# Performance work log

Measured on AMD Instinct MI355X. Metric: run time of the kernel, lower is better.

## Reference

```python
import jax, jax.numpy as jnp
import numpy as np

OUT_F, IN_F = 4096, 4096
BLOCK = 64  # bitsandbytes NF4 block size

# NF4 code table (bitsandbytes): 16 quantile levels of a standard normal, scaled to [-1, 1]
NF4_CODE = jnp.array([
    -1.0, -0.6961928009986877, -0.5250730514526367, -0.39491748809814453,
    -0.28444138169288635, -0.18477343022823334, -0.09105003625154495, 0.0,
    0.07958029955625534, 0.16093020141124725, 0.24611230194568634, 0.33791524171829224,
    0.44070982933044434, 0.5626170039176941, 0.7229568362236023, 1.0,
], dtype=jnp.float32)


def dequantize_nf4(packed, absmax):
    # packed: [OUT_F*IN_F//2] int values in [0,256); two 4-bit indices per byte (high nibble first)
    hi = (packed >> 4) & 0xF
    lo = packed & 0xF
    idx = jnp.stack([hi, lo], axis=-1).reshape(-1)           # [OUT_F*IN_F]
    vals = NF4_CODE[idx]                                      # lookup
    vals = vals.reshape(-1, BLOCK) * absmax[:, None]          # per-block scale
    return vals.reshape(OUT_F, IN_F)


def setup_inputs() -> dict:
    key = jax.random.key(0)
    k1, k2, k3, k4 = jax.random.split(key, 4)
    x = jax.random.normal(k1, (4, 2048, IN_F), dtype=jnp.float32)
    packed_weight = jax.random.randint(k2, (OUT_F * IN_F // 2,), 0, 256, dtype=jnp.int32)
    absmax = jax.random.uniform(k3, (OUT_F * IN_F // BLOCK,), dtype=jnp.float32)
    bias = jax.random.normal(k4, (OUT_F,), dtype=jnp.float32)
    return {"x": x, "packed_weight": packed_weight, "absmax": absmax, "bias": bias}


def reference(x, packed_weight, absmax, bias):
    weight = dequantize_nf4(packed_weight, absmax)            # [OUT_F, IN_F]
    # F.linear: x @ W^T + b
    return jnp.einsum('bsi,oi->bso', x, weight) + bias
```

## Files before the change

### kernel.cpp

```cpp
#include <hip/hip_runtime.h>
#include <hip/hip_bf16.h>
#include <stdint.h>

#define IN_F   4096
#define OUT_F  4096
#define MROWS  8192
#define NT     64

typedef __bf16 bf16x8 __attribute__((ext_vector_type(8)));
typedef float  f32x4  __attribute__((ext_vector_type(4)));
typedef unsigned short ushort8v __attribute__((ext_vector_type(8)));

__device__ __constant__ float NF4_TAB[16] = {
    -1.0f, -0.6961928009986877f, -0.5250730514526367f, -0.39491748809814453f,
    -0.28444138169288635f, -0.18477343022823334f, -0.09105003625154495f, 0.0f,
    0.07958029955625534f, 0.16093020141124725f, 0.24611230194568634f, 0.33791524171829224f,
    0.44070982933044434f, 0.5626170039176941f, 0.7229568362236023f, 1.0f,
};

__device__ __forceinline__ unsigned short f2bf_rne(float f) {
    unsigned u = __builtin_bit_cast(unsigned, f);
    return (unsigned short)((u + 0x7FFFu + ((u >> 16) & 1u)) >> 16);
}

__global__ __launch_bounds__(256) void prep_kernel(
        const float* __restrict__ x, const int* __restrict__ packed,
        const float* __restrict__ absmax,
        unsigned short* __restrict__ Wb, unsigned short* __restrict__ Xb) {
    __shared__ float tab[16];
    if (threadIdx.x < 16) tab[threadIdx.x] = NF4_TAB[threadIdx.x];
    __syncthreads();

    const int bid = blockIdx.x;
    if (bid < 512) {
        const int ngroups = OUT_F * IN_F / 8;
        const int stride = 512 * 256;
        for (int g = bid * 256 + threadIdx.x; g < ngroups; g += stride) {
            int4 pv = reinterpret_cast<const int4*>(packed)[g];
            float am = absmax[g >> 3];
            ushort8v o;
            o[0] = f2bf_rne(tab[(pv.x >> 4) & 0xF] * am);
            o[1] = f2bf_rne(tab[ pv.x       & 0xF] * am);
            o[2] = f2bf_rne(tab[(pv.y >> 4) & 0xF] * am);
            o[3] = f2bf_rne(tab[ pv.y       & 0xF] * am);
            o[4] = f2bf_rne(tab[(pv.z >> 4) & 0xF] * am);
            o[5] = f2bf_rne(tab[ pv.z       & 0xF] * am);
            o[6] = f2bf_rne(tab[(pv.w >> 4) & 0xF] * am);
            o[7] = f2bf_rne(tab[ pv.w       & 0xF] * am);
            *reinterpret_cast<ushort8v*>(&Wb[(size_t)g * 8]) = o;
        }
    } else {
        const int ngroups = MROWS * IN_F / 8;
        const int stride = 1536 * 256;
        for (int g = (bid - 512) * 256 + threadIdx.x; g < ngroups; g += stride) {
            float4 v0 = reinterpret_cast<const float4*>(x)[2 * g];
            float4 v1 = reinterpret_cast<const float4*>(x)[2 * g + 1];
            ushort8v o;
            o[0] = f2bf_rne(v0.x); o[1] = f2bf_rne(v0.y);
            o[2] = f2bf_rne(v0.z); o[3] = f2bf_rne(v0.w);
            o[4] = f2bf_rne(v1.x); o[5] = f2bf_rne(v1.y);
            o[6] = f2bf_rne(v1.z); o[7] = f2bf_rne(v1.w);
            *reinterpret_cast<ushort8v*>(&Xb[(size_t)g * 8]) = o;
        }
    }
}

#define GLOAD16(gp, lp)                                                        \
    __builtin_amdgcn_global_load_lds(                                          \
        (const __attribute__((address_space(1))) void*)(gp),                   \
        (__attribute__((address_space(3))) void*)(lp), 16, 0, 0)

#define BARF()  asm volatile("s_barrier" ::: "memory")
#define VMW(n)  asm volatile("s_waitcnt vmcnt(" #n ")" ::: "memory")

__global__ __launch_bounds__(512) void gemm256_kernel(
        const unsigned short* __restrict__ A,
        const unsigned short* __restrict__ B,
        const float* __restrict__ bias,
        float* __restrict__ C) {
    __shared__ __align__(16) unsigned short lds[65536];

    const int tid  = threadIdx.x;
    const int lane = tid & 63;
    const int wave = tid >> 6;
    const int wr   = wave >> 2;
    const int wcn  = wave & 3;
    const int lr   = lane & 15;
    const int lg   = lane >> 4;

    const int bid = blockIdx.x;
    const int wg  = (bid & 7) * 64 + (bid >> 3);
    const int bm  = (wg >> 4) << 8;
    const int bn  = (wg & 15) << 8;

    int srow[2], skel[2];
#pragma unroll
    for (int r = 0; r < 2; ++r) {
        int c = tid + r * 512;
        int L = c * 16;
        int sw = L ^ (((L >> 7) & 7) << 4);
        srow[r] = sw >> 6;
        skel[r] = (sw & 63) >> 1;
    }
    const unsigned short* pA0 = A + (size_t)(bm + srow[0]) * IN_F + skel[0];
    const unsigned short* pA1 = A + (size_t)(bm + srow[1]) * IN_F + skel[1];
    const unsigned short* pB0 = B + (size_t)(bn + srow[0]) * IN_F + skel[0];
    const unsigned short* pB1 = B + (size_t)(bn + srow[1]) * IN_F + skel[1];
    const int d0 = tid * 8, d1 = tid * 8 + 4096;

#define STAGE_A(t, kh) do {                                                    \
        int _b = ((t) & 1) * 32768 + (kh) * 8192;                              \
        int _k = (t) * 64 + (kh) * 32;                                         \
        GLOAD16(pA0 + _k, &lds[_b + d0]);                                      \
        GLOAD16(pA1 + _k, &lds[_b + d1]); } while (0)
#define STAGE_B(t, kh) do {                                                    \
        int _b = ((t) & 1) * 32768 + 16384 + (kh) * 8192;                      \
        int _k = (t) * 64 + (kh) * 32;                                         \
        GLOAD16(pB0 + _k, &lds[_b + d0]);                                      \
        GLOAD16(pB1 + _k, &lds[_b + d1]); } while (0)

    const int laneoff = ((lr * 64 + lg * 16) ^ (((lr >> 1) & 7) << 4)) >> 1;
    const int arow = wr * 128;
    const int brow = wcn * 64;

    f32x4  acc[8][4] = {};
    bf16x8 af[4], bfv[4];

#define LOADB(b, kh) do {                                                      \
        int _base = (b) * 32768 + 16384 + (kh) * 8192 + brow * 32 + laneoff;   \
        bfv[0] = *reinterpret_cast<const bf16x8*>(&lds[_base]);                \
        bfv[1] = *reinterpret_cast<const bf16x8*>(&lds[_base + 512]);          \
        bfv[2] = *reinterpret_cast<const bf16x8*>(&lds[_base + 1024]);         \
        bfv[3] = *reinterpret_cast<const bf16x8*>(&lds[_base + 1536]); } while (0)
#define LOADA(b, kh, mq) do {                                                  \
        int _base = (b) * 32768 + (kh) * 8192 + (arow + (mq) * 64) * 32 + laneoff; \
        af[0] = *reinterpret_cast<const bf16x8*>(&lds[_base]);                 \
        af[1] = *reinterpret_cast<const bf16x8*>(&lds[_base + 512]);           \
        af[2] = *reinterpret_cast<const bf16x8*>(&lds[_base + 1024]);          \
        af[3] = *reinterpret_cast<const bf16x8*>(&lds[_base + 1536]); } while (0)

#define MFMA16(mq) do {                                                        \
        __builtin_amdgcn_s_setprio(1);                                         \
        _Pragma("unroll")                                                      \
        for (int mi = 0; mi < 4; ++mi)                                         \
            _Pragma("unroll")                                                  \
            for (int ni = 0; ni < 4; ++ni)                                     \
                acc[(mq) * 4 + mi][ni] = __builtin_amdgcn_mfma_f32_16x16x32_bf16( \
                    af[mi], bfv[ni], acc[(mq) * 4 + mi][ni], 0, 0, 0);         \
        __builtin_amdgcn_s_setprio(0); } while (0)

#define PHASE1(b, S) do { LOADB(b, 0); LOADA(b, 0, 0); S;                      \
        MFMA16(0); BARF(); } while (0)
#define PHASE2(b, S) do { LOADA(b, 0, 1); S;                                   \
        MFMA16(1); BARF(); } while (0)
#define PHASE3(b, S) do { LOADB(b, 1); LOADA(b, 1, 0); S;                      \
        MFMA16(0); BARF(); } while (0)
#define PHASE4(b, S, V) do { LOADA(b, 1, 1); S;                                \
        MFMA16(1); V; BARF(); } while (0)

    STAGE_B(0, 0); STAGE_A(0, 0); STAGE_B(0, 1); STAGE_A(0, 1);
    STAGE_B(1, 0); STAGE_A(1, 0); STAGE_B(1, 1);
    VMW(6);
    BARF();

#pragma unroll 2
    for (int t = 0; t < NT - 2; ++t) {
        const int b = t & 1;
        PHASE1(b, STAGE_A(t + 1, 1));
        PHASE2(b, STAGE_B(t + 2, 0));
        PHASE3(b, STAGE_A(t + 2, 0));
        PHASE4(b, STAGE_B(t + 2, 1), VMW(6));
    }
    PHASE1(0, STAGE_A(NT - 1, 1));
    PHASE2(0, );
    PHASE3(0, );
    PHASE4(0, , VMW(0));
    PHASE1(1, );
    PHASE2(1, );
    PHASE3(1, );
    PHASE4(1, , );

#pragma unroll
    for (int a = 0; a < 8; ++a) {
        const int row0 = bm + wr * 128 + (a >> 2) * 64 + (a & 3) * 16 + lg * 4;
#pragma unroll
        for (int ni = 0; ni < 4; ++ni) {
            const int col = bn + wcn * 64 + ni * 16 + lr;
            const float bs = bias[col];
            float* cp = C + (size_t)row0 * OUT_F + col;
#pragma unroll
            for (int j = 0; j < 4; ++j)
                cp[(size_t)j * OUT_F] = acc[a][ni][j] + bs;
        }
    }
}

extern "C" void kernel_launch(void* const* d_in, const int* in_sizes, int n_in,
                              void* d_out, int out_size, void* d_ws, size_t ws_size,
                              hipStream_t stream) {
    const float* x      = (const float*)d_in[0];
    const int*   packed = (const int*)d_in[1];
    const float* absmax = (const float*)d_in[2];
    const float* bias   = (const float*)d_in[3];
    float* out = (float*)d_out;

    unsigned short* Wb = (unsigned short*)d_ws;
    unsigned short* Xb = Wb + (size_t)OUT_F * IN_F;

    prep_kernel<<<2048, 256, 0, stream>>>(x, packed, absmax, Wb, Xb);
    gemm256_kernel<<<512, 512, 0, stream>>>(Xb, Wb, bias, out);
}
```

Measured before the change: 482.0 us.

## Merge four MFMA phases into two per k-tile with dual A fragment registers

```diff
diff --git a/kernel.cpp b/kernel.cpp
--- a/kernel.cpp
+++ b/kernel.cpp
@@ -124,7 +124,7 @@
     const int brow = wcn * 64;
 
     f32x4  acc[8][4] = {};
-    bf16x8 af[4], bfv[4];
+    bf16x8 af0[4], af1[4], bfv[4];
 
 #define LOADB(b, kh) do {                                                      \
         int _base = (b) * 32768 + 16384 + (kh) * 8192 + brow * 32 + laneoff;   \
@@ -132,53 +132,48 @@
         bfv[1] = *reinterpret_cast<const bf16x8*>(&lds[_base + 512]);          \
         bfv[2] = *reinterpret_cast<const bf16x8*>(&lds[_base + 1024]);         \
         bfv[3] = *reinterpret_cast<const bf16x8*>(&lds[_base + 1536]); } while (0)
-#define LOADA(b, kh, mq) do {                                                  \
+#define LOADA(b, kh, mq, dst) do {                                             \
         int _base = (b) * 32768 + (kh) * 8192 + (arow + (mq) * 64) * 32 + laneoff; \
-        af[0] = *reinterpret_cast<const bf16x8*>(&lds[_base]);                 \
-        af[1] = *reinterpret_cast<const bf16x8*>(&lds[_base + 512]);           \
-        af[2] = *reinterpret_cast<const bf16x8*>(&lds[_base + 1024]);          \
-        af[3] = *reinterpret_cast<const bf16x8*>(&lds[_base + 1536]); } while (0)
-
-#define MFMA16(mq) do {                                                        \
+        dst[0] = *reinterpret_cast<const bf16x8*>(&lds[_base]);                \
+        dst[1] = *reinterpret_cast<const bf16x8*>(&lds[_base + 512]);          \
+        dst[2] = *reinterpret_cast<const bf16x8*>(&lds[_base + 1024]);         \
+        dst[3] = *reinterpret_cast<const bf16x8*>(&lds[_base + 1536]); } while (0)
+
+#define MFMA32() do {                                                          \
         __builtin_amdgcn_s_setprio(1);                                         \
         _Pragma("unroll")                                                      \
         for (int mi = 0; mi < 4; ++mi)                                         \
             _Pragma("unroll")                                                  \
             for (int ni = 0; ni < 4; ++ni)                                     \
-                acc[(mq) * 4 + mi][ni] = __builtin_amdgcn_mfma_f32_16x16x32_bf16( \
-                    af[mi], bfv[ni], acc[(mq) * 4 + mi][ni], 0, 0, 0);         \
+                acc[mi][ni] = __builtin_amdgcn_mfma_f32_16x16x32_bf16(         \
+                    af0[mi], bfv[ni], acc[mi][ni], 0, 0, 0);                   \
+        _Pragma("unroll")                                                      \
+        for (int mi = 0; mi < 4; ++mi)                                         \
+            _Pragma("unroll")                                                  \
+            for (int ni = 0; ni < 4; ++ni)                                     \
+                acc[4 + mi][ni] = __builtin_amdgcn_mfma_f32_16x16x32_bf16(     \
+                    af1[mi], bfv[ni], acc[4 + mi][ni], 0, 0, 0);               \
         __builtin_amdgcn_s_setprio(0); } while (0)
 
-#define PHASE1(b, S) do { LOADB(b, 0); LOADA(b, 0, 0); S;                      \
-        MFMA16(0); BARF(); } while (0)
-#define PHASE2(b, S) do { LOADA(b, 0, 1); S;                                   \
-        MFMA16(1); BARF(); } while (0)
-#define PHASE3(b, S) do { LOADB(b, 1); LOADA(b, 1, 0); S;                      \
-        MFMA16(0); BARF(); } while (0)
-#define PHASE4(b, S, V) do { LOADA(b, 1, 1); S;                                \
-        MFMA16(1); V; BARF(); } while (0)
-
-    STAGE_B(0, 0); STAGE_A(0, 0); STAGE_B(0, 1); STAGE_A(0, 1);
-    STAGE_B(1, 0); STAGE_A(1, 0); STAGE_B(1, 1);
+#define PHASE(b, kh, S1, S2, V) do {                                           \
+        LOADB(b, kh); LOADA(b, kh, 0, af0); LOADA(b, kh, 1, af1);              \
+        S1; S2; MFMA32(); V; BARF(); } while (0)
+
+    STAGE_A(0, 0); STAGE_B(0, 0); STAGE_A(0, 1);
+    STAGE_B(0, 1); STAGE_A(1, 0); STAGE_B(1, 0);
     VMW(6);
     BARF();
 
 #pragma unroll 2
     for (int t = 0; t < NT - 2; ++t) {
         const int b = t & 1;
-        PHASE1(b, STAGE_A(t + 1, 1));
-        PHASE2(b, STAGE_B(t + 2, 0));
-        PHASE3(b, STAGE_A(t + 2, 0));
-        PHASE4(b, STAGE_B(t + 2, 1), VMW(6));
-    }
-    PHASE1(0, STAGE_A(NT - 1, 1));
-    PHASE2(0, );
-    PHASE3(0, );
-    PHASE4(0, , VMW(0));
-    PHASE1(1, );
-    PHASE2(1, );
-    PHASE3(1, );
-    PHASE4(1, , );
+        PHASE(b, 0, STAGE_A(t + 1, 1), STAGE_B(t + 1, 1), VMW(6));
+        PHASE(b, 1, STAGE_A(t + 2, 0), STAGE_B(t + 2, 0), VMW(6));
+    }
+    PHASE(0, 0, STAGE_A(63, 1), STAGE_B(63, 1), VMW(6));
+    PHASE(0, 1, , , VMW(4));
+    PHASE(1, 0, , , VMW(0));
+    PHASE(1, 1, , , );
 
 #pragma unroll
     for (int a = 0; a < 8; ++a) {
```

Result: no change. 484.6 us (+0.6%).
